# Performance work log

Measured on AMD Instinct MI355X. Metric: run time of the kernel, lower is better.

## Reference

```python
import jax, jax.numpy as jnp
import numpy as np

B, L, D = 32, 2048, 1024


def setup_inputs() -> dict:
    key = jax.random.key(0)
    ks = jax.random.split(key, 8)
    s = 1.0 / np.sqrt(D).astype(np.float32)  # torch nn.Linear init scale
    return {
        "decoder_hidden": jax.random.normal(ks[0], (B, 1, D), jnp.float32),
        "encoder_outputs": jax.random.normal(ks[1], (B, L, D), jnp.float32),
        "W_w": jax.random.uniform(ks[2], (D, D), jnp.float32, -s, s),
        "W_b": jax.random.uniform(ks[3], (D,), jnp.float32, -s, s),
        "U_w": jax.random.uniform(ks[4], (D, D), jnp.float32, -s, s),
        "U_b": jax.random.uniform(ks[5], (D,), jnp.float32, -s, s),
        "v_w": jax.random.uniform(ks[6], (1, D), jnp.float32, -s, s),
        "v_b": jax.random.uniform(ks[7], (1,), jnp.float32, -s, s),
    }


def reference(decoder_hidden, encoder_outputs, W_w, W_b, U_w, U_b, v_w, v_b):
    # torch Linear: y = x @ W.T + b
    q = decoder_hidden @ W_w.T + W_b            # [B, 1, D]
    k = encoder_outputs @ U_w.T + U_b           # [B, L, D]
    scores = jnp.tanh(q + k) @ v_w.T + v_b      # [B, L, 1]
    attn = jax.nn.softmax(scores[..., 0], axis=-1)[:, None, :]  # [B, 1, L]
    context = jnp.einsum("bql,bld->bqd", attn, encoder_outputs)  # [B, 1, D]
    return (context, attn)
```

## Files before the change

kernel.cpp:

```cpp
#include <hip/hip_runtime.h>
#include <hip/hip_bf16.h>
#include <stdint.h>

#define BB 32
#define LL 2048
#define DD 1024

typedef short short8  __attribute__((ext_vector_type(8)));
typedef float f32x4   __attribute__((ext_vector_type(4)));

__device__ __forceinline__ short f2bf(float f) {
    unsigned u = __float_as_uint(f);
    u += 0x7fffu + ((u >> 16) & 1u);
    return (short)(u >> 16);
}

__device__ __forceinline__ float bf2f(unsigned short s) {
    return __uint_as_float(((unsigned)s) << 16);
}

__device__ __forceinline__ float fast_tanh(float x) {
    float e = __expf(2.f * x);
    return 1.f - 2.f * __builtin_amdgcn_rcpf(e + 1.f);
}

__device__ __forceinline__ void async_cp16(const void* g, void* l) {
    __builtin_amdgcn_global_load_lds(
        (__attribute__((address_space(1))) void*)g,
        (__attribute__((address_space(3))) void*)l, 16, 0, 0);
}

__device__ __forceinline__ short8 pack8(float4 a, float4 b) {
    short8 p;
    p[0] = f2bf(a.x); p[1] = f2bf(a.y); p[2] = f2bf(a.z); p[3] = f2bf(a.w);
    p[4] = f2bf(b.x); p[5] = f2bf(b.y); p[6] = f2bf(b.z); p[7] = f2bf(b.w);
    return p;
}

__global__ void prep_kernel(const float* __restrict__ dh, const float* __restrict__ Ww,
                            const float* __restrict__ Wb, const float* __restrict__ Ub,
                            const float* __restrict__ Uw, const float* __restrict__ enc,
                            float* __restrict__ qbuf, short* __restrict__ Ubf,
                            short* __restrict__ encbf) {
    const int bid = blockIdx.x, t = threadIdx.x;
    if (bid >= 512) {
        const float* src = (bid < 1024) ? Uw : enc;
        short* dst = (bid < 1024) ? Ubf : encbf;
        int base = (bid < 1024) ? (bid - 512) : (bid - 1024);
        size_t idx = ((size_t)base * 256 + t) * 8;
        float4 a = *(const float4*)(src + idx);
        float4 c = *(const float4*)(src + idx + 4);
        *(short8*)(dst + idx) = pack8(a, c);
        return;
    }
    int b  = bid >> 4;
    int d0 = (bid & 15) << 6;
    int w = t >> 6, lane = t & 63;
    __shared__ __align__(16) float hs[DD];
    *(float4*)&hs[t * 4] = *(const float4*)&dh[b * DD + t * 4];
    __syncthreads();
    float hr[16];
#pragma unroll
    for (int i = 0; i < 16; i++) hr[i] = hs[lane + 64 * i];
    for (int i = 0; i < 16; i++) {
        int d = d0 + w * 16 + i;
        const float* wr = Ww + (size_t)d * DD;
        float s = 0.f;
#pragma unroll
        for (int j = 0; j < 16; j++) s += wr[lane + 64 * j] * hr[j];
#pragma unroll
        for (int m = 1; m < 64; m <<= 1) s += __shfl_xor(s, m, 64);
        if (lane == 0) qbuf[b * DD + d] = s + Wb[d] + Ub[d];
    }
}

__global__ __launch_bounds__(256, 3) void gemm_scores_bf(
    const short* __restrict__ encbf, const short* __restrict__ Ubf,
    const float* __restrict__ qbuf, const float* __restrict__ vw,
    float* __restrict__ spart) {
    __shared__ __align__(16) short As[2][128 * 32];
    __shared__ __align__(16) short Bs[2][128 * 32];
    __shared__ float q_s[128], v_s[128], s_acc[2][128];

    const int t = threadIdx.x;
    const int lane = t & 63, w = t >> 6;
    const int l15 = lane & 15, quad = lane >> 4;
    const int wm = w >> 1, wn = w & 1;

    const int lin  = blockIdx.x + (blockIdx.y << 3);
    const int xcd  = lin & 7;
    const int slot = lin >> 3;
    const int nblk = slot & 7;
    const int mstripe = (xcd << 6) + (slot >> 3);
    const int n0 = nblk << 7;
    const int m0 = mstripe << 7;
    const int b  = m0 >> 11;

    if (t < 128) {
        q_s[t] = qbuf[(b << 10) + n0 + t];
        v_s[t] = vw[n0 + t];
    }

    f32x4 acc[4][4];
#pragma unroll
    for (int i = 0; i < 4; i++)
#pragma unroll
        for (int j = 0; j < 4; j++) acc[i][j] = (f32x4){0.f, 0.f, 0.f, 0.f};

    const int srow = lane >> 2, sseg = (lane & 3) << 3;
    const short* gA0 = encbf + (((size_t)(m0 + w * 32 + srow)) << 10) + sseg;
    const short* gB0 = Ubf   + (((size_t)(n0 + w * 32 + srow)) << 10) + sseg;
    const int lofs = w * 32 * 32;

    for (int k0 = 0; k0 < 1024; k0 += 64) {
        __syncthreads();
        async_cp16(gA0 + k0,                 &As[0][lofs]);
        async_cp16(gA0 + k0 + (16 << 10),    &As[0][lofs + 16 * 32]);
        async_cp16(gB0 + k0,                 &Bs[0][lofs]);
        async_cp16(gB0 + k0 + (16 << 10),    &Bs[0][lofs + 16 * 32]);
        async_cp16(gA0 + k0 + 32,            &As[1][lofs]);
        async_cp16(gA0 + k0 + 32 + (16 << 10), &As[1][lofs + 16 * 32]);
        async_cp16(gB0 + k0 + 32,            &Bs[1][lofs]);
        async_cp16(gB0 + k0 + 32 + (16 << 10), &Bs[1][lofs + 16 * 32]);
        __syncthreads();

#pragma unroll
        for (int h = 0; h < 2; h++) {
            short8 af[4], bfv[4];
#pragma unroll
            for (int mt = 0; mt < 4; mt++)
                af[mt] = *(const short8*)&As[h][(wm * 64 + mt * 16 + l15) * 32 + quad * 8];
#pragma unroll
            for (int nt = 0; nt < 4; nt++)
                bfv[nt] = *(const short8*)&Bs[h][(wn * 64 + nt * 16 + l15) * 32 + quad * 8];
#pragma unroll
            for (int mt = 0; mt < 4; mt++)
#pragma unroll
                for (int nt = 0; nt < 4; nt++)
                    acc[mt][nt] = __builtin_amdgcn_mfma_f32_16x16x32_bf16(
                        af[mt], bfv[nt], acc[mt][nt], 0, 0, 0);
        }
    }

    float qn[4], vn[4];
#pragma unroll
    for (int nt = 0; nt < 4; nt++) {
        qn[nt] = q_s[wn * 64 + nt * 16 + l15];
        vn[nt] = v_s[wn * 64 + nt * 16 + l15];
    }
#pragma unroll
    for (int mt = 0; mt < 4; mt++) {
#pragma unroll
        for (int r = 0; r < 4; r++) {
            float sum = 0.f;
#pragma unroll
            for (int nt = 0; nt < 4; nt++)
                sum += vn[nt] * fast_tanh(acc[mt][nt][r] + qn[nt]);
            sum += __shfl_xor(sum, 1, 64);
            sum += __shfl_xor(sum, 2, 64);
            sum += __shfl_xor(sum, 4, 64);
            sum += __shfl_xor(sum, 8, 64);
            if (l15 == 0)
                s_acc[wn][wm * 64 + mt * 16 + quad * 4 + r] = sum;
        }
    }
    __syncthreads();
    if (t < 128)
        spart[((size_t)nblk << 16) + m0 + t] = s_acc[0][t] + s_acc[1][t];
}

__global__ void softmax8_kernel(const float* __restrict__ sp, float* __restrict__ attn) {
    const int b = blockIdx.x, t = threadIdx.x;
    const int w = t >> 6, lane = t & 63;
    __shared__ float rm[4], rs[4];
    float v[8];
#pragma unroll
    for (int i = 0; i < 8; i++) {
        int l = t + (i << 8);
        float s = 0.f;
#pragma unroll
        for (int p = 0; p < 8; p++) s += sp[(p << 16) + (b << 11) + l];
        v[i] = s;
    }
    float m = v[0];
#pragma unroll
    for (int i = 1; i < 8; i++) m = fmaxf(m, v[i]);
#pragma unroll
    for (int s = 1; s < 64; s <<= 1) m = fmaxf(m, __shfl_xor(m, s, 64));
    if (lane == 0) rm[w] = m;
    __syncthreads();
    m = fmaxf(fmaxf(rm[0], rm[1]), fmaxf(rm[2], rm[3]));
    float s = 0.f;
#pragma unroll
    for (int i = 0; i < 8; i++) { v[i] = __expf(v[i] - m); s += v[i]; }
#pragma unroll
    for (int k = 1; k < 64; k <<= 1) s += __shfl_xor(s, k, 64);
    if (lane == 0) rs[w] = s;
    __syncthreads();
    s = rs[0] + rs[1] + rs[2] + rs[3];
    float inv = 1.f / s;
#pragma unroll
    for (int i = 0; i < 8; i++) attn[(b << 11) + t + (i << 8)] = v[i] * inv;
}

__global__ void ctx_part(const short* __restrict__ encbf, const float* __restrict__ attn,
                         float* __restrict__ ctx) {
    const int dchunk = blockIdx.x;
    const int lslab  = blockIdx.y;
    const int b      = blockIdx.z;
    const int t = threadIdx.x;
    __shared__ float at_s[256];
    __shared__ float red[8][128];
    at_s[t] = attn[(b << 11) + (lslab << 8) + t];
    __syncthreads();
    const int d4 = (t & 31) << 2;
    const int dl = t >> 5;
    const int d0 = dchunk << 7;
    const short* base = encbf + ((size_t)b << 21) + ((size_t)lslab << 18) + d0 + d4;
    float ax = 0.f, ay = 0.f, az = 0.f, aw = 0.f;
#pragma unroll 8
    for (int i = 0; i < 32; i++) {
        int l = (i << 3) + dl;
        float wg = at_s[l];
        ushort4 e = *(const ushort4*)(base + ((size_t)l << 10));
        ax += wg * bf2f(e.x); ay += wg * bf2f(e.y);
        az += wg * bf2f(e.z); aw += wg * bf2f(e.w);
    }
    red[dl][d4 + 0] = ax;
    red[dl][d4 + 1] = ay;
    red[dl][d4 + 2] = az;
    red[dl][d4 + 3] = aw;
    __syncthreads();
    if (t < 128) {
        float s = 0.f;
#pragma unroll
        for (int j = 0; j < 8; j++) s += red[j][t];
        atomicAdd(&ctx[(b << 10) + d0 + t], s);
    }
}

__global__ void cvt_bf16_kernel(const float* __restrict__ src, short* __restrict__ dst) {
    int idx = (blockIdx.x * 256 + threadIdx.x) * 8;
    float4 a = *(const float4*)(src + idx);
    float4 c = *(const float4*)(src + idx + 4);
    *(short8*)(dst + idx) = pack8(a, c);
}

__global__ void q_kernel(const float* __restrict__ dh, const float* __restrict__ Ww,
                         const float* __restrict__ Wb, const float* __restrict__ Ub,
                         float* __restrict__ qbuf) {
    int b  = blockIdx.x >> 4;
    int d0 = (blockIdx.x & 15) << 6;
    int t = threadIdx.x, w = t >> 6, lane = t & 63;
    __shared__ __align__(16) float hs[DD];
    *(float4*)&hs[t * 4] = *(const float4*)&dh[b * DD + t * 4];
    __syncthreads();
    float hr[16];
#pragma unroll
    for (int i = 0; i < 16; i++) hr[i] = hs[lane + 64 * i];
    for (int i = 0; i < 16; i++) {
        int d = d0 + w * 16 + i;
        const float* wr = Ww + (size_t)d * DD;
        float s = 0.f;
#pragma unroll
        for (int j = 0; j < 16; j++) s += wr[lane + 64 * j] * hr[j];
#pragma unroll
        for (int m = 1; m < 64; m <<= 1) s += __shfl_xor(s, m, 64);
        if (lane == 0) qbuf[b * DD + d] = s + Wb[d] + Ub[d];
    }
}

__global__ __launch_bounds__(256, 3) void gemm_scores_f32(
    const float* __restrict__ enc, const short* __restrict__ Ubf,
    const float* __restrict__ qbuf, const float* __restrict__ vw,
    float* __restrict__ scores) {
    __shared__ __align__(16) short As[128 * 32];
    __shared__ __align__(16) short Bs[128 * 32];
    __shared__ float q_s[128], v_s[128], s_acc[128];

    const int t = threadIdx.x;
    const int lane = t & 63, w = t >> 6;
    const int l15 = lane & 15, quad = lane >> 4;
    const int wm = w >> 1, wn = w & 1;
    const int n0 = blockIdx.x << 7;
    const int m0 = blockIdx.y << 7;
    const int b  = m0 >> 11;

    if (t < 128) {
        q_s[t] = qbuf[(b << 10) + n0 + t];
        v_s[t] = vw[n0 + t];
        s_acc[t] = 0.f;
    }

    f32x4 acc[4][4];
#pragma unroll
    for (int i = 0; i < 4; i++)
#pragma unroll
        for (int j = 0; j < 4; j++) acc[i][j] = (f32x4){0.f, 0.f, 0.f, 0.f};

    const int arow = t >> 1, ahalf = t & 1;
    const float* aptr = enc + (((size_t)(m0 + arow)) << 10) + (ahalf << 4);
    short* adst = As + arow * 32 + ahalf * 16;
    const int brow = t >> 2, bks = (t & 3) * 8;
    const short* bptr1 = Ubf + ((size_t)(n0 + brow)) * 1024 + bks;
    const short* bptr2 = bptr1 + (size_t)64 * 1024;
    short* bdst1 = Bs + brow * 32 + bks;
    short* bdst2 = bdst1 + 64 * 32;

    for (int k0 = 0; k0 < 1024; k0 += 32) {
        __syncthreads();
        float4 f0 = *(const float4*)(aptr + k0);
        float4 f1 = *(const float4*)(aptr + k0 + 4);
        float4 f2 = *(const float4*)(aptr + k0 + 8);
        float4 f3 = *(const float4*)(aptr + k0 + 12);
        *(short8*)adst = pack8(f0, f1);
        *(short8*)(adst + 8) = pack8(f2, f3);
        *(short8*)bdst1 = *(const short8*)(bptr1 + k0);
        *(short8*)bdst2 = *(const short8*)(bptr2 + k0);
        __syncthreads();

        short8 af[4], bfv[4];
#pragma unroll
        for (int mt = 0; mt < 4; mt++)
            af[mt] = *(const short8*)&As[(wm * 64 + mt * 16 + l15) * 32 + quad * 8];
#pragma unroll
        for (int nt = 0; nt < 4; nt++)
            bfv[nt] = *(const short8*)&Bs[(wn * 64 + nt * 16 + l15) * 32 + quad * 8];
#pragma unroll
        for (int mt = 0; mt < 4; mt++)
#pragma unroll
            for (int nt = 0; nt < 4; nt++)
                acc[mt][nt] = __builtin_amdgcn_mfma_f32_16x16x32_bf16(
                    af[mt], bfv[nt], acc[mt][nt], 0, 0, 0);
    }

    float qn[4], vn[4];
#pragma unroll
    for (int nt = 0; nt < 4; nt++) {
        qn[nt] = q_s[wn * 64 + nt * 16 + l15];
        vn[nt] = v_s[wn * 64 + nt * 16 + l15];
    }
#pragma unroll
    for (int mt = 0; mt < 4; mt++) {
#pragma unroll
        for (int r = 0; r < 4; r++) {
            float sum = 0.f;
#pragma unroll
            for (int nt = 0; nt < 4; nt++)
                sum += vn[nt] * fast_tanh(acc[mt][nt][r] + qn[nt]);
            sum += __shfl_xor(sum, 1, 64);
            sum += __shfl_xor(sum, 2, 64);
            sum += __shfl_xor(sum, 4, 64);
            sum += __shfl_xor(sum, 8, 64);
            if (l15 == 0)
                atomicAdd(&s_acc[wm * 64 + mt * 16 + quad * 4 + r], sum);
        }
    }
    __syncthreads();
    if (t < 128) atomicAdd(&scores[m0 + t], s_acc[t]);
}

__global__ void softmax_kernel(const float* __restrict__ sp, float* __restrict__ attn) {
    int b = blockIdx.x, t = threadIdx.x;
    int w = t >> 6, lane = t & 63;
    __shared__ float rm[4], rs[4];
    float v[8];
#pragma unroll
    for (int i = 0; i < 8; i++) v[i] = sp[(b << 11) + t + (i << 8)];
    float m = v[0];
#pragma unroll
    for (int i = 1; i < 8; i++) m = fmaxf(m, v[i]);
#pragma unroll
    for (int s = 1; s < 64; s <<= 1) m = fmaxf(m, __shfl_xor(m, s, 64));
    if (lane == 0) rm[w] = m;
    __syncthreads();
    m = fmaxf(fmaxf(rm[0], rm[1]), fmaxf(rm[2], rm[3]));
    float s = 0.f;
#pragma unroll
    for (int i = 0; i < 8; i++) { v[i] = __expf(v[i] - m); s += v[i]; }
#pragma unroll
    for (int k = 1; k < 64; k <<= 1) s += __shfl_xor(s, k, 64);
    if (lane == 0) rs[w] = s;
    __syncthreads();
    s = rs[0] + rs[1] + rs[2] + rs[3];
    float inv = 1.f / s;
#pragma unroll
    for (int i = 0; i < 8; i++) attn[(b << 11) + t + (i << 8)] = v[i] * inv;
}

__global__ void context_f32(const float* __restrict__ enc, const float* __restrict__ attn,
                            float* __restrict__ ctx) {
    int dchunk = blockIdx.x, b = blockIdx.y;
    int t = threadIdx.x;
    __shared__ __align__(16) float at_s[2048];
    __shared__ float red[16][128];
    *(float4*)&at_s[t * 4] = *(const float4*)&attn[(b << 11) + t * 4];
    __syncthreads();
    int d4 = (t & 31) << 2;
    int dl = t >> 5;
    int d0 = dchunk << 7;
    const float* base = enc + ((size_t)b << 21) + d0 + d4;
    float ax = 0.f, ay = 0.f, az = 0.f, aw = 0.f;
#pragma unroll 4
    for (int i = 0; i < 128; i++) {
        int l = (i << 4) + dl;
        float wg = at_s[l];
        float4 e = *(const float4*)(base + ((size_t)l << 10));
        ax += wg * e.x; ay += wg * e.y; az += wg * e.z; aw += wg * e.w;
    }
    red[dl][d4 + 0] = ax;
    red[dl][d4 + 1] = ay;
    red[dl][d4 + 2] = az;
    red[dl][d4 + 3] = aw;
    __syncthreads();
    if (t < 128) {
        float s = 0.f;
#pragma unroll
        for (int j = 0; j < 16; j++) s += red[j][t];
        ctx[(b << 10) + d0 + t] = s;
    }
}

extern "C" void kernel_launch(void* const* d_in, const int* in_sizes, int n_in,
                              void* d_out, int out_size, void* d_ws, size_t ws_size,
                              hipStream_t stream) {
    const float* dh  = (const float*)d_in[0];
    const float* enc = (const float*)d_in[1];
    const float* Ww  = (const float*)d_in[2];
    const float* Wb  = (const float*)d_in[3];
    const float* Uw  = (const float*)d_in[4];
    const float* Ub  = (const float*)d_in[5];
    const float* vw  = (const float*)d_in[6];

    float* out  = (float*)d_out;
    float* attn = out + BB * DD;
    char*  ws   = (char*)d_ws;
    short* Ubf   = (short*)ws;
    float* qbuf  = (float*)(ws + (2 << 20));
    float* sbuf  = (float*)(ws + (2 << 20) + (1 << 17));
    short* encbf = (short*)(ws + (8 << 20));

    bool bigws = ws_size >= ((size_t)143 << 20);

    if (bigws) {
        hipMemsetAsync(out, 0, (size_t)BB * DD * sizeof(float), stream);
        prep_kernel<<<33792, 256, 0, stream>>>(dh, Ww, Wb, Ub, Uw, enc, qbuf, Ubf, encbf);
        gemm_scores_bf<<<dim3(8, 512), 256, 0, stream>>>(encbf, Ubf, qbuf, vw, sbuf);
        softmax8_kernel<<<BB, 256, 0, stream>>>(sbuf, attn);
        ctx_part<<<dim3(8, 8, BB), 256, 0, stream>>>(encbf, attn, out);
    } else {
        hipMemsetAsync(sbuf, 0, (size_t)BB * LL * sizeof(float), stream);
        cvt_bf16_kernel<<<512, 256, 0, stream>>>(Uw, Ubf);
        q_kernel<<<512, 256, 0, stream>>>(dh, Ww, Wb, Ub, qbuf);
        gemm_scores_f32<<<dim3(8, 512), 256, 0, stream>>>(enc, Ubf, qbuf, vw, sbuf);
        softmax_kernel<<<BB, 256, 0, stream>>>(sbuf, attn);
        context_f32<<<dim3(8, BB), 512, 0, stream>>>(enc, attn, out);
    }
}
```

Baseline: 563.6 us.

## Software-pipeline GEMM K-loop with double-buffered async loads and raise occupancy

```diff
diff --git a/kernel.cpp b/kernel.cpp
--- a/kernel.cpp
+++ b/kernel.cpp
@@ -74,7 +74,7 @@
     }
 }
 
-__global__ __launch_bounds__(256, 3) void gemm_scores_bf(
+__global__ __launch_bounds__(256, 4) void gemm_scores_bf(
     const short* __restrict__ encbf, const short* __restrict__ Ubf,
     const float* __restrict__ qbuf, const float* __restrict__ vw,
     float* __restrict__ spart) {
@@ -112,34 +112,39 @@
     const short* gB0 = Ubf   + (((size_t)(n0 + w * 32 + srow)) << 10) + sseg;
     const int lofs = w * 32 * 32;
 
-    for (int k0 = 0; k0 < 1024; k0 += 64) {
+    auto stage = [&](int buf, int k) {
+        async_cp16(gA0 + k,              &As[buf][lofs]);
+        async_cp16(gA0 + k + (16 << 10), &As[buf][lofs + 512]);
+        async_cp16(gB0 + k,              &Bs[buf][lofs]);
+        async_cp16(gB0 + k + (16 << 10), &Bs[buf][lofs + 512]);
+    };
+    auto compute = [&](int buf) {
+        short8 af[4], bfv[4];
+#pragma unroll
+        for (int mt = 0; mt < 4; mt++)
+            af[mt] = *(const short8*)&As[buf][(wm * 64 + mt * 16 + l15) * 32 + quad * 8];
+#pragma unroll
+        for (int nt = 0; nt < 4; nt++)
+            bfv[nt] = *(const short8*)&Bs[buf][(wn * 64 + nt * 16 + l15) * 32 + quad * 8];
+#pragma unroll
+        for (int mt = 0; mt < 4; mt++)
+#pragma unroll
+            for (int nt = 0; nt < 4; nt++)
+                acc[mt][nt] = __builtin_amdgcn_mfma_f32_16x16x32_bf16(
+                    af[mt], bfv[nt], acc[mt][nt], 0, 0, 0);
+    };
+
+    stage(0, 0);
+    __syncthreads();
+
+    for (int it = 0; it < 16; ++it) {
+        stage(1, (it << 6) + 32);
+        compute(0);
         __syncthreads();
-        async_cp16(gA0 + k0,                 &As[0][lofs]);
-        async_cp16(gA0 + k0 + (16 << 10),    &As[0][lofs + 16 * 32]);
-        async_cp16(gB0 + k0,                 &Bs[0][lofs]);
-        async_cp16(gB0 + k0 + (16 << 10),    &Bs[0][lofs + 16 * 32]);
-        async_cp16(gA0 + k0 + 32,            &As[1][lofs]);
-        async_cp16(gA0 + k0 + 32 + (16 << 10), &As[1][lofs + 16 * 32]);
-        async_cp16(gB0 + k0 + 32,            &Bs[1][lofs]);
-        async_cp16(gB0 + k0 + 32 + (16 << 10), &Bs[1][lofs + 16 * 32]);
+        if (it < 15)
+            stage(0, (it << 6) + 64);
+        compute(1);
         __syncthreads();
-
-#pragma unroll
-        for (int h = 0; h < 2; h++) {
-            short8 af[4], bfv[4];
-#pragma unroll
-            for (int mt = 0; mt < 4; mt++)
-                af[mt] = *(const short8*)&As[h][(wm * 64 + mt * 16 + l15) * 32 + quad * 8];
-#pragma unroll
-            for (int nt = 0; nt < 4; nt++)
-                bfv[nt] = *(const short8*)&Bs[h][(wn * 64 + nt * 16 + l15) * 32 + quad * 8];
-#pragma unroll
-            for (int mt = 0; mt < 4; mt++)
-#pragma unroll
-                for (int nt = 0; nt < 4; nt++)
-                    acc[mt][nt] = __builtin_amdgcn_mfma_f32_16x16x32_bf16(
-                        af[mt], bfv[nt], acc[mt][nt], 0, 0, 0);
-        }
     }
 
     float qn[4], vn[4];
```

New measurement: 586.7 us. +4.1%, slower.

## Triple-buffer GEMM K-slabs with async prefetch and XOR-swizzled LDS layout

Applied to the files above, without the earlier changes.

```diff
diff --git a/kernel.cpp b/kernel.cpp
--- a/kernel.cpp
+++ b/kernel.cpp
@@ -78,8 +78,8 @@
     const short* __restrict__ encbf, const short* __restrict__ Ubf,
     const float* __restrict__ qbuf, const float* __restrict__ vw,
     float* __restrict__ spart) {
-    __shared__ __align__(16) short As[2][128 * 32];
-    __shared__ __align__(16) short Bs[2][128 * 32];
+    __shared__ __align__(16) short As[3 * 128 * 32];
+    __shared__ __align__(16) short Bs[3 * 128 * 32];
     __shared__ float q_s[128], v_s[128], s_acc[2][128];
 
     const int t = threadIdx.x;
@@ -107,40 +107,56 @@
 #pragma unroll
         for (int j = 0; j < 4; j++) acc[i][j] = (f32x4){0.f, 0.f, 0.f, 0.f};
 
-    const int srow = lane >> 2, sseg = (lane & 3) << 3;
-    const short* gA0 = encbf + (((size_t)(m0 + w * 32 + srow)) << 10) + sseg;
-    const short* gB0 = Ubf   + (((size_t)(n0 + w * 32 + srow)) << 10) + sseg;
-    const int lofs = w * 32 * 32;
-
-    for (int k0 = 0; k0 < 1024; k0 += 64) {
-        __syncthreads();
-        async_cp16(gA0 + k0,                 &As[0][lofs]);
-        async_cp16(gA0 + k0 + (16 << 10),    &As[0][lofs + 16 * 32]);
-        async_cp16(gB0 + k0,                 &Bs[0][lofs]);
-        async_cp16(gB0 + k0 + (16 << 10),    &Bs[0][lofs + 16 * 32]);
-        async_cp16(gA0 + k0 + 32,            &As[1][lofs]);
-        async_cp16(gA0 + k0 + 32 + (16 << 10), &As[1][lofs + 16 * 32]);
-        async_cp16(gB0 + k0 + 32,            &Bs[1][lofs]);
-        async_cp16(gB0 + k0 + 32 + (16 << 10), &Bs[1][lofs + 16 * 32]);
-        __syncthreads();
-
-#pragma unroll
-        for (int h = 0; h < 2; h++) {
-            short8 af[4], bfv[4];
-#pragma unroll
-            for (int mt = 0; mt < 4; mt++)
-                af[mt] = *(const short8*)&As[h][(wm * 64 + mt * 16 + l15) * 32 + quad * 8];
+    const int srow  = lane >> 2;
+    const int sslot = ((lane & 3) ^ ((lane >> 3) & 3)) << 3;
+    const short* gA0 = encbf + (((size_t)(m0 + w * 32 + srow)) << 10) + sslot;
+    const short* gB0 = Ubf   + (((size_t)(n0 + w * 32 + srow)) << 10) + sslot;
+    const int lofs = w * 1024;
+    const int qsw = (quad ^ ((l15 >> 1) & 3)) << 3;
+
+    auto stageSlab = [&](int buf, int k) {
+        short* la = As + buf * 4096 + lofs;
+        short* lb = Bs + buf * 4096 + lofs;
+        async_cp16(gA0 + k,               la);
+        async_cp16(gA0 + k + (16 << 10),  la + 512);
+        async_cp16(gB0 + k,               lb);
+        async_cp16(gB0 + k + (16 << 10),  lb + 512);
+    };
+
+    stageSlab(0, 0);
+    stageSlab(1, 32);
+    asm volatile("s_waitcnt vmcnt(4)" ::: "memory");
+    __builtin_amdgcn_s_barrier();
+    __builtin_amdgcn_sched_barrier(0);
+
+    int rb = 0, sb = 2;
+    for (int j = 0; j < 32; ++j) {
+        const short* Ab = As + rb * 4096;
+        const short* Bb = Bs + rb * 4096;
+        short8 af[4], bfv[4];
+#pragma unroll
+        for (int mt = 0; mt < 4; mt++)
+            af[mt] = *(const short8*)&Ab[(wm * 64 + mt * 16 + l15) * 32 + qsw];
+#pragma unroll
+        for (int nt = 0; nt < 4; nt++)
+            bfv[nt] = *(const short8*)&Bb[(wn * 64 + nt * 16 + l15) * 32 + qsw];
+        if (j < 30) stageSlab(sb, (j + 2) << 5);
+#pragma unroll
+        for (int mt = 0; mt < 4; mt++)
 #pragma unroll
             for (int nt = 0; nt < 4; nt++)
-                bfv[nt] = *(const short8*)&Bs[h][(wn * 64 + nt * 16 + l15) * 32 + quad * 8];
-#pragma unroll
-            for (int mt = 0; mt < 4; mt++)
-#pragma unroll
-                for (int nt = 0; nt < 4; nt++)
-                    acc[mt][nt] = __builtin_amdgcn_mfma_f32_16x16x32_bf16(
-                        af[mt], bfv[nt], acc[mt][nt], 0, 0, 0);
+                acc[mt][nt] = __builtin_amdgcn_mfma_f32_16x16x32_bf16(
+                    af[mt], bfv[nt], acc[mt][nt], 0, 0, 0);
+        if (j < 31) {
+            if (j < 30) asm volatile("s_waitcnt vmcnt(4)" ::: "memory");
+            else        asm volatile("s_waitcnt vmcnt(0)" ::: "memory");
+            __builtin_amdgcn_s_barrier();
+            __builtin_amdgcn_sched_barrier(0);
         }
-    }
+        rb = (rb == 2) ? 0 : rb + 1;
+        sb = (sb == 2) ? 0 : sb + 1;
+    }
+    __syncthreads();
 
     float qn[4], vn[4];
 #pragma unroll
```

After: 584.7 us. +3.7%, slower.

## Rework bf16 score GEMM into 256x256 tiles with pipelined, swizzled LDS loads

Applied to the files above, without the earlier changes.

```diff
diff --git a/kernel.cpp b/kernel.cpp
--- a/kernel.cpp
+++ b/kernel.cpp
@@ -74,82 +74,159 @@
     }
 }
 
-__global__ __launch_bounds__(256, 3) void gemm_scores_bf(
+__global__ __launch_bounds__(512, 2) void gemm_scores_bf(
     const short* __restrict__ encbf, const short* __restrict__ Ubf,
     const float* __restrict__ qbuf, const float* __restrict__ vw,
     float* __restrict__ spart) {
-    __shared__ __align__(16) short As[2][128 * 32];
-    __shared__ __align__(16) short Bs[2][128 * 32];
-    __shared__ float q_s[128], v_s[128], s_acc[2][128];
+    __shared__ __align__(16) short As[256 * 64];
+    __shared__ __align__(16) short Bs[256 * 64];
+    __shared__ float q_s[256], v_s[256];
+    __shared__ float s_acc[4][256];
 
     const int t = threadIdx.x;
-    const int lane = t & 63, w = t >> 6;
+    const int lane = t & 63, wid = t >> 6;
     const int l15 = lane & 15, quad = lane >> 4;
-    const int wm = w >> 1, wn = w & 1;
-
-    const int lin  = blockIdx.x + (blockIdx.y << 3);
+    const int wm = wid >> 2, wn = wid & 3;
+
+    const int lin  = blockIdx.x + (blockIdx.y << 2);
     const int xcd  = lin & 7;
     const int slot = lin >> 3;
-    const int nblk = slot & 7;
-    const int mstripe = (xcd << 6) + (slot >> 3);
-    const int n0 = nblk << 7;
-    const int m0 = mstripe << 7;
+    const int nblk = slot & 3;
+    const int mstripe = (xcd << 5) + (slot >> 2);
+    const int n0 = nblk << 8;
+    const int m0 = mstripe << 8;
     const int b  = m0 >> 11;
 
-    if (t < 128) {
+    if (t < 256) {
         q_s[t] = qbuf[(b << 10) + n0 + t];
         v_s[t] = vw[n0 + t];
     }
 
-    f32x4 acc[4][4];
-#pragma unroll
-    for (int i = 0; i < 4; i++)
+    f32x4 acc[8][4];
+#pragma unroll
+    for (int i = 0; i < 8; i++)
 #pragma unroll
         for (int j = 0; j < 4; j++) acc[i][j] = (f32x4){0.f, 0.f, 0.f, 0.f};
 
-    const int srow = lane >> 2, sseg = (lane & 3) << 3;
-    const short* gA0 = encbf + (((size_t)(m0 + w * 32 + srow)) << 10) + sseg;
-    const short* gB0 = Ubf   + (((size_t)(n0 + w * 32 + srow)) << 10) + sseg;
-    const int lofs = w * 32 * 32;
-
-    for (int k0 = 0; k0 < 1024; k0 += 64) {
-        __syncthreads();
-        async_cp16(gA0 + k0,                 &As[0][lofs]);
-        async_cp16(gA0 + k0 + (16 << 10),    &As[0][lofs + 16 * 32]);
-        async_cp16(gB0 + k0,                 &Bs[0][lofs]);
-        async_cp16(gB0 + k0 + (16 << 10),    &Bs[0][lofs + 16 * 32]);
-        async_cp16(gA0 + k0 + 32,            &As[1][lofs]);
-        async_cp16(gA0 + k0 + 32 + (16 << 10), &As[1][lofs + 16 * 32]);
-        async_cp16(gB0 + k0 + 32,            &Bs[1][lofs]);
-        async_cp16(gB0 + k0 + 32 + (16 << 10), &Bs[1][lofs + 16 * 32]);
-        __syncthreads();
-
-#pragma unroll
-        for (int h = 0; h < 2; h++) {
-            short8 af[4], bfv[4];
-#pragma unroll
-            for (int mt = 0; mt < 4; mt++)
-                af[mt] = *(const short8*)&As[h][(wm * 64 + mt * 16 + l15) * 32 + quad * 8];
-#pragma unroll
-            for (int nt = 0; nt < 4; nt++)
-                bfv[nt] = *(const short8*)&Bs[h][(wn * 64 + nt * 16 + l15) * 32 + quad * 8];
-#pragma unroll
-            for (int mt = 0; mt < 4; mt++)
-#pragma unroll
-                for (int nt = 0; nt < 4; nt++)
-                    acc[mt][nt] = __builtin_amdgcn_mfma_f32_16x16x32_bf16(
-                        af[mt], bfv[nt], acc[mt][nt], 0, 0, 0);
+    const int grow = t >> 3;
+    const int gseg = ((t & 7) ^ ((t >> 3) & 7)) << 3;
+    const short* gA = encbf + (((size_t)(m0 + grow)) << 10) + gseg;
+    const short* gB = Ubf   + (((size_t)(n0 + grow)) << 10) + gseg;
+    short* const lA = As + (wid << 9);
+    short* const lB = Bs + (wid << 9);
+
+    const int swz0 = ((quad)     ^ (l15 & 7)) << 3;
+    const int swz1 = ((4 + quad) ^ (l15 & 7)) << 3;
+    const int arow = (((wm << 7) + l15)) << 6;
+    const int brow = (((wn << 6) + l15)) << 6;
+
+#define STA(i, k0) async_cp16(gA + ((size_t)(i) << 16) + (k0), lA + ((i) << 12))
+#define STB(i, k0) async_cp16(gB + ((size_t)(i) << 16) + (k0), lB + ((i) << 12))
+
+    STA(0, 0); STA(1, 0); STA(2, 0); STA(3, 0);
+    STB(0, 0); STB(1, 0); STB(2, 0); STB(3, 0);
+    asm volatile("s_waitcnt vmcnt(0)" ::: "memory");
+    __builtin_amdgcn_s_barrier();
+    __builtin_amdgcn_sched_barrier(0);
+
+    short8 a_[4][2], b0_[2][2], b1_[2][2];
+
+    for (int kt = 0; kt < 16; ++kt) {
+        const int k1 = (kt + 1) << 6;
+        const bool st = kt < 15;
+
+#pragma unroll
+        for (int m = 0; m < 4; m++) {
+            a_[m][0] = *(const short8*)&As[arow + (m << 10) + swz0];
+            a_[m][1] = *(const short8*)&As[arow + (m << 10) + swz1];
         }
-    }
+#pragma unroll
+        for (int n = 0; n < 2; n++) {
+            b0_[n][0] = *(const short8*)&Bs[brow + (n << 10) + swz0];
+            b0_[n][1] = *(const short8*)&Bs[brow + (n << 10) + swz1];
+        }
+        asm volatile("s_waitcnt lgkmcnt(0)" ::: "memory");
+        __builtin_amdgcn_sched_barrier(0);
+        __builtin_amdgcn_s_setprio(1);
+#pragma unroll
+        for (int m = 0; m < 4; m++)
+#pragma unroll
+            for (int n = 0; n < 2; n++) {
+                acc[m][n] = __builtin_amdgcn_mfma_f32_16x16x32_bf16(a_[m][0], b0_[n][0], acc[m][n], 0, 0, 0);
+                acc[m][n] = __builtin_amdgcn_mfma_f32_16x16x32_bf16(a_[m][1], b0_[n][1], acc[m][n], 0, 0, 0);
+            }
+        __builtin_amdgcn_s_setprio(0);
+        __builtin_amdgcn_s_barrier();
+        __builtin_amdgcn_sched_barrier(0);
+
+#pragma unroll
+        for (int n = 0; n < 2; n++) {
+            b1_[n][0] = *(const short8*)&Bs[brow + ((n + 2) << 10) + swz0];
+            b1_[n][1] = *(const short8*)&Bs[brow + ((n + 2) << 10) + swz1];
+        }
+        if (st) { STA(0, k1); STA(2, k1); }
+        asm volatile("s_waitcnt lgkmcnt(0)" ::: "memory");
+        __builtin_amdgcn_sched_barrier(0);
+        __builtin_amdgcn_s_setprio(1);
+#pragma unroll
+        for (int m = 0; m < 4; m++)
+#pragma unroll
+            for (int n = 0; n < 2; n++) {
+                acc[m][n + 2] = __builtin_amdgcn_mfma_f32_16x16x32_bf16(a_[m][0], b1_[n][0], acc[m][n + 2], 0, 0, 0);
+                acc[m][n + 2] = __builtin_amdgcn_mfma_f32_16x16x32_bf16(a_[m][1], b1_[n][1], acc[m][n + 2], 0, 0, 0);
+            }
+        __builtin_amdgcn_s_setprio(0);
+        if (st) asm volatile("s_waitcnt vmcnt(2)" ::: "memory");
+        else    asm volatile("s_waitcnt vmcnt(0)" ::: "memory");
+        __builtin_amdgcn_s_barrier();
+        __builtin_amdgcn_sched_barrier(0);
+
+#pragma unroll
+        for (int m = 0; m < 4; m++) {
+            a_[m][0] = *(const short8*)&As[arow + ((m + 4) << 10) + swz0];
+            a_[m][1] = *(const short8*)&As[arow + ((m + 4) << 10) + swz1];
+        }
+        if (st) { STB(0, k1); STB(1, k1); STB(2, k1); STB(3, k1); }
+        asm volatile("s_waitcnt lgkmcnt(0)" ::: "memory");
+        __builtin_amdgcn_sched_barrier(0);
+        __builtin_amdgcn_s_setprio(1);
+#pragma unroll
+        for (int m = 0; m < 4; m++)
+#pragma unroll
+            for (int n = 0; n < 2; n++) {
+                acc[m + 4][n + 2] = __builtin_amdgcn_mfma_f32_16x16x32_bf16(a_[m][0], b1_[n][0], acc[m + 4][n + 2], 0, 0, 0);
+                acc[m + 4][n + 2] = __builtin_amdgcn_mfma_f32_16x16x32_bf16(a_[m][1], b1_[n][1], acc[m + 4][n + 2], 0, 0, 0);
+            }
+        __builtin_amdgcn_s_setprio(0);
+        __builtin_amdgcn_s_barrier();
+        __builtin_amdgcn_sched_barrier(0);
+
+        if (st) { STA(1, k1); STA(3, k1); }
+        __builtin_amdgcn_s_setprio(1);
+#pragma unroll
+        for (int m = 0; m < 4; m++)
+#pragma unroll
+            for (int n = 0; n < 2; n++) {
+                acc[m + 4][n] = __builtin_amdgcn_mfma_f32_16x16x32_bf16(a_[m][0], b0_[n][0], acc[m + 4][n], 0, 0, 0);
+                acc[m + 4][n] = __builtin_amdgcn_mfma_f32_16x16x32_bf16(a_[m][1], b0_[n][1], acc[m + 4][n], 0, 0, 0);
+            }
+        __builtin_amdgcn_s_setprio(0);
+        if (st) asm volatile("s_waitcnt vmcnt(2)" ::: "memory");
+        else    asm volatile("s_waitcnt vmcnt(0)" ::: "memory");
+        __builtin_amdgcn_s_barrier();
+        __builtin_amdgcn_sched_barrier(0);
+    }
+#undef STA
+#undef STB
 
     float qn[4], vn[4];
 #pragma unroll
     for (int nt = 0; nt < 4; nt++) {
-        qn[nt] = q_s[wn * 64 + nt * 16 + l15];
-        vn[nt] = v_s[wn * 64 + nt * 16 + l15];
-    }
-#pragma unroll
-    for (int mt = 0; mt < 4; mt++) {
+        qn[nt] = q_s[(wn << 6) + nt * 16 + l15];
+        vn[nt] = v_s[(wn << 6) + nt * 16 + l15];
+    }
+#pragma unroll
+    for (int mt = 0; mt < 8; mt++) {
 #pragma unroll
         for (int r = 0; r < 4; r++) {
             float sum = 0.f;
@@ -161,12 +238,13 @@
             sum += __shfl_xor(sum, 4, 64);
             sum += __shfl_xor(sum, 8, 64);
             if (l15 == 0)
-                s_acc[wn][wm * 64 + mt * 16 + quad * 4 + r] = sum;
+                s_acc[wn][(wm << 7) + mt * 16 + (quad << 2) + r] = sum;
         }
     }
     __syncthreads();
-    if (t < 128)
-        spart[((size_t)nblk << 16) + m0 + t] = s_acc[0][t] + s_acc[1][t];
+    if (t < 256)
+        spart[((size_t)nblk << 16) + m0 + t] =
+            s_acc[0][t] + s_acc[1][t] + s_acc[2][t] + s_acc[3][t];
 }
 
 __global__ void softmax8_kernel(const float* __restrict__ sp, float* __restrict__ attn) {
@@ -179,7 +257,7 @@
         int l = t + (i << 8);
         float s = 0.f;
 #pragma unroll
-        for (int p = 0; p < 8; p++) s += sp[(p << 16) + (b << 11) + l];
+        for (int p = 0; p < 4; p++) s += sp[(p << 16) + (b << 11) + l];
         v[i] = s;
     }
     float m = v[0];
@@ -445,7 +523,7 @@
     if (bigws) {
         hipMemsetAsync(out, 0, (size_t)BB * DD * sizeof(float), stream);
         prep_kernel<<<33792, 256, 0, stream>>>(dh, Ww, Wb, Ub, Uw, enc, qbuf, Ubf, encbf);
-        gemm_scores_bf<<<dim3(8, 512), 256, 0, stream>>>(encbf, Ubf, qbuf, vw, sbuf);
+        gemm_scores_bf<<<dim3(4, 256), 512, 0, stream>>>(encbf, Ubf, qbuf, vw, sbuf);
         softmax8_kernel<<<BB, 256, 0, stream>>>(sbuf, attn);
         ctx_part<<<dim3(8, 8, BB), 256, 0, stream>>>(encbf, attn, out);
     } else {
```

Result: slower. 578.4 us (+2.6%).
